# Kernel tuning notes

Hardware: AMD Instinct MI355X
Metric: run time of the kernel (lower is better)

Reference implementation:

```python
import jax, jax.numpy as jnp
import numpy as np

D = 256          # num_channels
H = 4            # num_heads
DH = D // H      # head dim
BN_EPS = 1e-5


def conv1x1(x, W, b):
    # x: [B, Cin, N], W: [Cout, Cin], b: [Cout] -> [B, Cout, N]
    return jnp.einsum('oc,bcn->bon', W, x) + b[None, :, None]


def bn_eval(x, gamma, beta):
    # eval-mode BatchNorm1d with running_mean=0, running_var=1
    scale = gamma / jnp.sqrt(1.0 + BN_EPS)
    return x * scale[None, :, None] + beta[None, :, None]


def setup_inputs() -> dict:
    key = jax.random.key(0)
    ks = jax.random.split(key, 16)
    B, N = 1, 4096
    s = 0.05
    inp = {
        'corr_feat_belief': jax.random.normal(ks[0], (B, D, N), dtype=jnp.float32),
        'spatial_compatibility': jax.random.uniform(ks[1], (B, N, N), dtype=jnp.float32),
        'Wq': jax.random.normal(ks[2], (D, D), dtype=jnp.float32) * s,
        'bq': jnp.zeros((D,), jnp.float32),
        'Wk': jax.random.normal(ks[3], (D, D), dtype=jnp.float32) * s,
        'bk': jnp.zeros((D,), jnp.float32),
        'Wv': jax.random.normal(ks[4], (D, D), dtype=jnp.float32) * s,
        'bv': jnp.zeros((D,), jnp.float32),
        'W1': jax.random.normal(ks[5], (D // 2, D), dtype=jnp.float32) * s,
        'b1': jnp.zeros((D // 2,), jnp.float32),
        'g1': jnp.ones((D // 2,), jnp.float32),
        'be1': jnp.zeros((D // 2,), jnp.float32),
        'W2': jax.random.normal(ks[6], (D // 2, D // 2), dtype=jnp.float32) * s,
        'b2': jnp.zeros((D // 2,), jnp.float32),
        'g2': jnp.ones((D // 2,), jnp.float32),
        'be2': jnp.zeros((D // 2,), jnp.float32),
        'W3': jax.random.normal(ks[7], (D, D // 2), dtype=jnp.float32) * s,
        'b3': jnp.zeros((D,), jnp.float32),
    }
    return inp


def reference(corr_feat_belief, spatial_compatibility, Wq, bq, Wk, bk, Wv, bv,
              W1, b1, g1, be1, W2, b2, g2, be2, W3, b3):
    x = corr_feat_belief                      # [B, D, N]
    B, _, N = x.shape
    # QKV conv1x1 projections, split heads -> [B, H, DH, N]
    Q = conv1x1(x, Wq, bq).reshape(B, H, DH, N)
    K = conv1x1(x, Wk, bk).reshape(B, H, DH, N)
    V = conv1x1(x, Wv, bv).reshape(B, H, DH, N)
    # attention scores [B, H, N, N], scaled
    att = jnp.einsum('bhco,bhci->bhoi', Q, K) / np.sqrt(DH).astype(np.float32)
    # multiplicative spatial-compatibility mask, softmax over keys
    weight = jax.nn.softmax(spatial_compatibility[:, None, :, :] * att, axis=-1)
    message = jnp.einsum('bhoi,bhci->bhco', weight, V).reshape(B, D, N)
    # message MLP: conv1x1 -> BN -> ReLU -> conv1x1 -> BN -> ReLU -> conv1x1
    h = jax.nn.relu(bn_eval(conv1x1(message, W1, b1), g1, be1))
    h = jax.nn.relu(bn_eval(conv1x1(h, W2, b2), g2, be2))
    h = conv1x1(h, W3, b3)
    return x + h
```

## Files before the change

kernel.cpp:

```cpp
#include <hip/hip_runtime.h>
#include <hip/hip_bf16.h>
#include <math.h>

#define D_CH   256
#define NHEAD  4
#define DHEAD  64
#define NPTS   4096
#define KSPLIT 8
#define KCHUNK (NPTS / KSPLIT)
#define BN_RSQ 0.99999500003749963f
#define HSTRIDE 262144

typedef __attribute__((ext_vector_type(4))) float f32x4;
typedef __attribute__((ext_vector_type(8))) short bf16x8;
typedef unsigned short ushort_t;

__device__ __forceinline__ ushort_t f2bf(float x) {
    unsigned int b = __float_as_uint(x);
    return (ushort_t)((b + 0x7FFF + ((b >> 16) & 1)) >> 16);
}
__device__ __forceinline__ float bf2f(ushort_t u) {
    return __uint_as_float(((unsigned int)u) << 16);
}
__device__ __forceinline__ unsigned cvt_pk(float lo, float hi) {
    unsigned r;
    asm("v_cvt_pk_bf16_f32 %0, %1, %2" : "=v"(r) : "v"(lo), "v"(hi));
    return r;
}

__global__ __launch_bounds__(256) void transpose_cast(
    const float* __restrict__ x, ushort_t* __restrict__ xT)
{
    __shared__ float xs[64][65];
    const int tid = threadIdx.x;
    const int n0 = blockIdx.x * 64, k0 = blockIdx.y * 64;
#pragma unroll
    for (int p = 0; p < 16; ++p) {
        int kk = p * 4 + (tid >> 6), nn = tid & 63;
        xs[kk][nn] = x[(size_t)(k0 + kk) * NPTS + n0 + nn];
    }
    __syncthreads();
#pragma unroll
    for (int p = 0; p < 16; ++p) {
        int nn = p * 4 + (tid >> 6), kk = tid & 63;
        xT[(size_t)(n0 + nn) * D_CH + k0 + kk] = f2bf(xs[kk][nn]);
    }
}

__device__ __forceinline__ void gemm_tile_body(
    const float* __restrict__ A, const ushort_t* __restrict__ Bt,
    int K, int m0, int n0, int l15, int lhi, f32x4 acc[2][2])
{
#pragma unroll
    for (int i = 0; i < 2; ++i)
#pragma unroll
        for (int j = 0; j < 2; ++j) acc[i][j] = (f32x4){0.f, 0.f, 0.f, 0.f};

    for (int k0 = 0; k0 < K; k0 += 32) {
        bf16x8 af[2], bfr[2];
#pragma unroll
        for (int mf = 0; mf < 2; ++mf) {
            const float* ap = A + (size_t)(m0 + mf * 16 + l15) * K + k0 + lhi * 8;
            float4 a0 = *(const float4*)ap;
            float4 a1 = *(const float4*)(ap + 4);
            unsigned* tp = (unsigned*)&af[mf];
            tp[0] = cvt_pk(a0.x, a0.y);
            tp[1] = cvt_pk(a0.z, a0.w);
            tp[2] = cvt_pk(a1.x, a1.y);
            tp[3] = cvt_pk(a1.z, a1.w);
        }
#pragma unroll
        for (int nf = 0; nf < 2; ++nf)
            bfr[nf] = *(const bf16x8*)&Bt[(size_t)(n0 + nf * 16 + l15) * K + k0 + lhi * 8];
#pragma unroll
        for (int mf = 0; mf < 2; ++mf)
#pragma unroll
            for (int nf = 0; nf < 2; ++nf)
                acc[mf][nf] = __builtin_amdgcn_mfma_f32_16x16x32_bf16(af[mf], bfr[nf], acc[mf][nf], 0, 0, 0);
    }
}

__global__ __launch_bounds__(256) void gemm_qkv(
    const float* __restrict__ Wq, const float* __restrict__ bq,
    const float* __restrict__ Wk, const float* __restrict__ bk,
    const float* __restrict__ Wv, const float* __restrict__ bv,
    const ushort_t* __restrict__ xT,
    ushort_t* __restrict__ Qf, ushort_t* __restrict__ Kf, ushort_t* __restrict__ Vf)
{
    const int tid = threadIdx.x;
    const int w = tid >> 6, lane = tid & 63, l15 = lane & 15, lhi = lane >> 4;
    const int wm = w >> 1, wn = w & 1;
    const int m0 = blockIdx.y * 64 + wm * 32;
    const int n0 = blockIdx.x * 64 + wn * 32;
    const int z = blockIdx.z;

    const float* A    = (z == 0) ? Wq : (z == 1) ? Wk : Wv;
    const float* bias = (z == 0) ? bq : (z == 1) ? bk : bv;
    ushort_t* dst     = (z == 0) ? Qf : (z == 1) ? Kf : Vf;
    const float scl   = (z == 0) ? 0.125f : 1.0f;

    f32x4 acc[2][2];
    gemm_tile_body(A, xT, D_CH, m0, n0, l15, lhi, acc);

#pragma unroll
    for (int mf = 0; mf < 2; ++mf) {
#pragma unroll
        for (int r = 0; r < 4; ++r) {
            int m = m0 + mf * 16 + lhi * 4 + r;
            int head = m >> 6, dch = m & 63;
            float bi = bias[m];
#pragma unroll
            for (int nf = 0; nf < 2; ++nf) {
                int n = n0 + nf * 16 + l15;
                float v = (acc[mf][nf][r] + bi) * scl;
                size_t idx;
                if (z < 2)
                    idx = (size_t)head * HSTRIDE + (size_t)(n >> 4) * 1024 + (dch >> 5) * 512
                        + (((dch >> 3) & 3) * 16 + (n & 15)) * 8 + (dch & 7);
                else
                    idx = (size_t)head * HSTRIDE + (size_t)(n >> 6) * 4096 + (dch >> 4) * 1024
                        + ((n >> 5) & 1) * 512 + (((n >> 3) & 3) * 16 + (dch & 15)) * 8 + (n & 7);
                dst[idx] = (ushort_t)(cvt_pk(v, v) & 0xFFFF);
            }
        }
    }
}

__global__ __launch_bounds__(256) void gemm_mfma32(
    const float* __restrict__ A, const ushort_t* __restrict__ Bt,
    void* __restrict__ Cout, int M, int N, int K,
    const float* __restrict__ bias, const float* __restrict__ gamma,
    const float* __restrict__ beta, int relu, const float* __restrict__ resid,
    int out_mode)
{
    const int tid = threadIdx.x;
    const int w = tid >> 6, lane = tid & 63, l15 = lane & 15, lhi = lane >> 4;
    const int wm = w >> 1, wn = w & 1;
    const int m0 = blockIdx.y * 32 + wm * 16;
    const int n0 = blockIdx.x * 64 + wn * 32;

    f32x4 acc[2];
#pragma unroll
    for (int j = 0; j < 2; ++j) acc[j] = (f32x4){0.f, 0.f, 0.f, 0.f};

    for (int k0 = 0; k0 < K; k0 += 32) {
        const float* ap = A + (size_t)(m0 + l15) * K + k0 + lhi * 8;
        float4 a0 = *(const float4*)ap;
        float4 a1 = *(const float4*)(ap + 4);
        bf16x8 af;
        unsigned* tp = (unsigned*)&af;
        tp[0] = cvt_pk(a0.x, a0.y);
        tp[1] = cvt_pk(a0.z, a0.w);
        tp[2] = cvt_pk(a1.x, a1.y);
        tp[3] = cvt_pk(a1.z, a1.w);
#pragma unroll
        for (int nf = 0; nf < 2; ++nf) {
            bf16x8 bfr = *(const bf16x8*)&Bt[(size_t)(n0 + nf * 16 + l15) * K + k0 + lhi * 8];
            acc[nf] = __builtin_amdgcn_mfma_f32_16x16x32_bf16(af, bfr, acc[nf], 0, 0, 0);
        }
    }

    float* Cf = (float*)Cout;
    ushort_t* Cu = (ushort_t*)Cout;
#pragma unroll
    for (int r = 0; r < 4; ++r) {
        int m = m0 + lhi * 4 + r;
        float bi = bias[m];
        float sc = 1.0f, sh = 0.0f;
        if (gamma) { sc = gamma[m] * BN_RSQ; sh = beta[m]; }
#pragma unroll
        for (int nf = 0; nf < 2; ++nf) {
            int n = n0 + nf * 16 + l15;
            float v = acc[nf][r] + bi;
            if (gamma) v = v * sc + sh;
            if (relu)  v = fmaxf(v, 0.0f);
            if (resid) v += resid[(size_t)m * N + n];
            if (out_mode == 0) Cf[(size_t)m * N + n] = v;
            else               Cu[(size_t)n * M + m] = (ushort_t)(cvt_pk(v, v) & 0xFFFF);
        }
    }
}

__device__ __forceinline__ void attn_tile(
    int kt, int ktn, const float* __restrict__ Sg,
    const ushort_t* __restrict__ Kh, const ushort_t* __restrict__ Vh,
    const bf16x8 (&qf)[2][2],
    ushort_t (* __restrict__ Sw)[72],
    f32x4 (&macc)[2][4], float (&lrun)[2],
    ushort_t (* __restrict__ Pw)[72], int l15, int lhi, int lane)
{
    f32x4 sr[8];
#pragma unroll
    for (int p = 0; p < 8; ++p)
        sr[p] = *(const f32x4*)&Sg[(size_t)p * 4 * NPTS + (size_t)ktn * 64];

    f32x4 sacc0[4], sacc1[4];
    __builtin_amdgcn_s_setprio(1);
#pragma unroll
    for (int kb = 0; kb < 4; ++kb) {
        const ushort_t* kp = Kh + (size_t)(kt * 4 + kb) * 1024 + lane * 8;
        bf16x8 kf0 = *(const bf16x8*)kp;
        bf16x8 kf1 = *(const bf16x8*)(kp + 512);
        f32x4 z0 = (f32x4){0.f, 0.f, 0.f, 0.f};
        z0 = __builtin_amdgcn_mfma_f32_16x16x32_bf16(kf0, qf[0][0], z0, 0, 0, 0);
        z0 = __builtin_amdgcn_mfma_f32_16x16x32_bf16(kf1, qf[0][1], z0, 0, 0, 0);
        sacc0[kb] = z0;
        f32x4 z1 = (f32x4){0.f, 0.f, 0.f, 0.f};
        z1 = __builtin_amdgcn_mfma_f32_16x16x32_bf16(kf0, qf[1][0], z1, 0, 0, 0);
        z1 = __builtin_amdgcn_mfma_f32_16x16x32_bf16(kf1, qf[1][1], z1, 0, 0, 0);
        sacc1[kb] = z1;
    }
    __builtin_amdgcn_s_setprio(0);

    bf16x8 vf[8];
    const ushort_t* vb = Vh + (size_t)kt * 4096 + lane * 8;
#pragma unroll
    for (int mm = 0; mm < 2; ++mm)
#pragma unroll
        for (int db = 0; db < 4; ++db)
            vf[mm * 4 + db] = *(const bf16x8*)(vb + db * 1024 + mm * 512);

    float ts0 = 0.0f, ts1 = 0.0f;
#pragma unroll
    for (int kb = 0; kb < 4; ++kb) {
        unsigned a0 = *(const unsigned*)&Sw[l15][kb * 16 + lhi * 4];
        unsigned a1 = *(const unsigned*)&Sw[l15][kb * 16 + lhi * 4 + 2];
        unsigned b0 = *(const unsigned*)&Sw[16 + l15][kb * 16 + lhi * 4];
        unsigned b1 = *(const unsigned*)&Sw[16 + l15][kb * 16 + lhi * 4 + 2];
        float p00 = __expf(sacc0[kb][0] * bf2f((ushort_t)(a0 & 0xFFFF)));
        float p01 = __expf(sacc0[kb][1] * bf2f((ushort_t)(a0 >> 16)));
        float p02 = __expf(sacc0[kb][2] * bf2f((ushort_t)(a1 & 0xFFFF)));
        float p03 = __expf(sacc0[kb][3] * bf2f((ushort_t)(a1 >> 16)));
        float p10 = __expf(sacc1[kb][0] * bf2f((ushort_t)(b0 & 0xFFFF)));
        float p11 = __expf(sacc1[kb][1] * bf2f((ushort_t)(b0 >> 16)));
        float p12 = __expf(sacc1[kb][2] * bf2f((ushort_t)(b1 & 0xFFFF)));
        float p13 = __expf(sacc1[kb][3] * bf2f((ushort_t)(b1 >> 16)));
        ts0 += (p00 + p01) + (p02 + p03);
        ts1 += (p10 + p11) + (p12 + p13);
        *(unsigned*)&Pw[l15][kb * 16 + lhi * 4]          = cvt_pk(p00, p01);
        *(unsigned*)&Pw[l15][kb * 16 + lhi * 4 + 2]      = cvt_pk(p02, p03);
        *(unsigned*)&Pw[16 + l15][kb * 16 + lhi * 4]     = cvt_pk(p10, p11);
        *(unsigned*)&Pw[16 + l15][kb * 16 + lhi * 4 + 2] = cvt_pk(p12, p13);
    }
    lrun[0] += ts0;
    lrun[1] += ts1;

#pragma unroll
    for (int p = 0; p < 8; ++p) {
        *(unsigned*)&Sw[p * 4 + lhi][l15 * 4]     = cvt_pk(sr[p][0], sr[p][1]);
        *(unsigned*)&Sw[p * 4 + lhi][l15 * 4 + 2] = cvt_pk(sr[p][2], sr[p][3]);
    }

    __builtin_amdgcn_s_setprio(1);
#pragma unroll
    for (int mm = 0; mm < 2; ++mm) {
        bf16x8 pf0 = *(const bf16x8*)&Pw[l15][mm * 32 + lhi * 8];
        bf16x8 pf1 = *(const bf16x8*)&Pw[16 + l15][mm * 32 + lhi * 8];
#pragma unroll
        for (int db = 0; db < 4; ++db) {
            macc[0][db] = __builtin_amdgcn_mfma_f32_16x16x32_bf16(vf[mm * 4 + db], pf0, macc[0][db], 0, 0, 0);
            macc[1][db] = __builtin_amdgcn_mfma_f32_16x16x32_bf16(vf[mm * 4 + db], pf1, macc[1][db], 0, 0, 0);
        }
    }
    __builtin_amdgcn_s_setprio(0);
}

__global__ __launch_bounds__(256, 3) void attn_mfma(
    const ushort_t* __restrict__ Qf, const ushort_t* __restrict__ Kf,
    const ushort_t* __restrict__ Vf, const float* __restrict__ S,
    ushort_t* __restrict__ pacc, float* __restrict__ pl)
{
    __shared__ __align__(16) ushort_t P_lds[4][32][72];
    __shared__ __align__(16) ushort_t S_lds[4][32][72];

    const int tid  = threadIdx.x;
    const int w    = tid >> 6;
    const int lane = tid & 63;
    const int l15  = lane & 15;
    const int lhi  = lane >> 4;
    const int h    = blockIdx.y;
    const int ks   = blockIdx.z;
    const int q0   = blockIdx.x * 128 + w * 32;
    const int ktb  = ks * (KCHUNK / 64);

    const ushort_t* Kh = Kf + (size_t)h * HSTRIDE;
    const ushort_t* Vh = Vf + (size_t)h * HSTRIDE;
    const float* Sg = S + (size_t)(q0 + lhi) * NPTS + l15 * 4;
    ushort_t (* __restrict__ Pw)[72] = P_lds[w];
    ushort_t (* __restrict__ Sw)[72] = S_lds[w];

    bf16x8 qf[2][2];
#pragma unroll
    for (int f = 0; f < 2; ++f) {
        const ushort_t* qp = Qf + (size_t)h * HSTRIDE
                           + (size_t)((q0 + f * 16) >> 4) * 1024 + lane * 8;
        qf[f][0] = *(const bf16x8*)qp;
        qf[f][1] = *(const bf16x8*)(qp + 512);
    }

    f32x4 macc[2][4];
#pragma unroll
    for (int f = 0; f < 2; ++f)
#pragma unroll
        for (int db = 0; db < 4; ++db) macc[f][db] = (f32x4){0.f, 0.f, 0.f, 0.f};
    float lrun[2] = {0.0f, 0.0f};

    {
#pragma unroll
        for (int p = 0; p < 8; ++p) {
            f32x4 t = *(const f32x4*)&Sg[(size_t)p * 4 * NPTS + (size_t)ktb * 64];
            *(unsigned*)&Sw[p * 4 + lhi][l15 * 4]     = cvt_pk(t[0], t[1]);
            *(unsigned*)&Sw[p * 4 + lhi][l15 * 4 + 2] = cvt_pk(t[2], t[3]);
        }
    }

    for (int kt = ktb; kt < ktb + 8; ++kt) {
        const int ktn = (kt + 1 < ktb + 8) ? kt + 1 : ktb;
        attn_tile(kt, ktn, Sg, Kh, Vh, qf, Sw, macc, lrun, Pw, l15, lhi, lane);
    }

#pragma unroll
    for (int f = 0; f < 2; ++f) {
        lrun[f] += __shfl_xor(lrun[f], 16);
        lrun[f] += __shfl_xor(lrun[f], 32);
    }

    const size_t pb = ((size_t)ks * NHEAD + h) * NPTS;
#pragma unroll
    for (int f = 0; f < 2; ++f) {
        ushort_t* prow = pacc + (pb + q0 + f * 16 + l15) * DHEAD;
#pragma unroll
        for (int db = 0; db < 4; ++db) {
            *(unsigned*)&prow[db * 16 + lhi * 4]     = cvt_pk(macc[f][db][0], macc[f][db][1]);
            *(unsigned*)&prow[db * 16 + lhi * 4 + 2] = cvt_pk(macc[f][db][2], macc[f][db][3]);
        }
    }
    if (lane < 16) {
        pl[pb + q0 + lane]      = lrun[0];
        pl[pb + q0 + 16 + lane] = lrun[1];
    }
}

__global__ __launch_bounds__(256) void attn_merge(
    const ushort_t* __restrict__ pacc, const float* __restrict__ pl,
    ushort_t* __restrict__ msgT)
{
    const int h = blockIdx.y;
    const int q = blockIdx.x * 64 + (threadIdx.x >> 2);
    const int d0 = (threadIdx.x & 3) * 16;

    float ls = 0.0f;
#pragma unroll
    for (int ks = 0; ks < KSPLIT; ++ks)
        ls += pl[((size_t)ks * NHEAD + h) * NPTS + q];
    float inv = 1.0f / ls;

    float out[16];
#pragma unroll
    for (int j = 0; j < 16; ++j) out[j] = 0.0f;
#pragma unroll
    for (int ks = 0; ks < KSPLIT; ++ks) {
        const ushort_t* ap = pacc + (((size_t)ks * NHEAD + h) * NPTS + q) * DHEAD + d0;
        bf16x8 v0 = *(const bf16x8*)ap;
        bf16x8 v1 = *(const bf16x8*)(ap + 8);
#pragma unroll
        for (int j = 0; j < 8; ++j) {
            out[j]     += bf2f((ushort_t)v0[j]);
            out[8 + j] += bf2f((ushort_t)v1[j]);
        }
    }
    unsigned o[8];
#pragma unroll
    for (int j = 0; j < 4; ++j) {
        o[j]     = cvt_pk(out[j * 2] * inv,     out[j * 2 + 1] * inv);
        o[4 + j] = cvt_pk(out[8 + j * 2] * inv, out[8 + j * 2 + 1] * inv);
    }
    unsigned* op = (unsigned*)(msgT + (size_t)q * D_CH + h * DHEAD + d0);
    *(uint4*)op       = make_uint4(o[0], o[1], o[2], o[3]);
    *(uint4*)(op + 4) = make_uint4(o[4], o[5], o[6], o[7]);
}

extern "C" void kernel_launch(void* const* d_in, const int* in_sizes, int n_in,
                              void* d_out, int out_size, void* d_ws, size_t ws_size,
                              hipStream_t stream) {
    const float* x  = (const float*)d_in[0];
    const float* S  = (const float*)d_in[1];
    const float* Wq = (const float*)d_in[2];
    const float* bq = (const float*)d_in[3];
    const float* Wk = (const float*)d_in[4];
    const float* bk = (const float*)d_in[5];
    const float* Wv = (const float*)d_in[6];
    const float* bv = (const float*)d_in[7];
    const float* W1 = (const float*)d_in[8];
    const float* b1 = (const float*)d_in[9];
    const float* g1 = (const float*)d_in[10];
    const float* be1= (const float*)d_in[11];
    const float* W2 = (const float*)d_in[12];
    const float* b2 = (const float*)d_in[13];
    const float* g2 = (const float*)d_in[14];
    const float* be2= (const float*)d_in[15];
    const float* W3 = (const float*)d_in[16];
    const float* b3 = (const float*)d_in[17];

    char* ws = (char*)d_ws;
    const size_t MB = 1024 * 1024;
    ushort_t* xT   = (ushort_t*)(ws);
    ushort_t* Qf   = (ushort_t*)(ws + 2 * MB);
    ushort_t* Kf   = (ushort_t*)(ws + 4 * MB);
    ushort_t* Vf   = (ushort_t*)(ws + 6 * MB);
    ushort_t* pacc = (ushort_t*)(ws + 8 * MB);
    float*    pl   = (float*)   (ws + 24 * MB);
    ushort_t* msgT = (ushort_t*)(ws + 25 * MB);
    ushort_t* h1T  = (ushort_t*)(ws + 27 * MB);
    ushort_t* h2T  = (ushort_t*)(ws + 28 * MB);

    transpose_cast<<<dim3(64, 4), 256, 0, stream>>>(x, xT);
    gemm_qkv<<<dim3(64, 4, 3), 256, 0, stream>>>(Wq, bq, Wk, bk, Wv, bv, xT, Qf, Kf, Vf);

    attn_mfma<<<dim3(32, NHEAD, KSPLIT), 256, 0, stream>>>(Qf, Kf, Vf, S, pacc, pl);
    attn_merge<<<dim3(64, NHEAD), 256, 0, stream>>>(pacc, pl, msgT);

    gemm_mfma32<<<dim3(64, 4), 256, 0, stream>>>(W1, msgT, h1T, 128, NPTS, 256, b1, g1, be1, 1, nullptr, 3);
    gemm_mfma32<<<dim3(64, 4), 256, 0, stream>>>(W2, h1T, h2T, 128, NPTS, 128, b2, g2, be2, 1, nullptr, 3);
    gemm_mfma32<<<dim3(64, 8), 256, 0, stream>>>(W3, h2T, d_out, 256, NPTS, 128, b3, nullptr, nullptr, 0, x, 0);
}
```

Baseline: 101.7 us.

## Fuse three MLP conv1x1 GEMMs into a single per-point-block kernel

Replaces three separate GEMM launches for the message MLP with one kernel in which each block processes 32 points through all three layers. Intermediate activations are still written to global scratch, but they are read back by the same block after a block barrier, so they stay cache-local. This removes two kernel launches and inter-kernel gaps, at the cost of only 128 blocks and serialized layers within a block.

```diff
diff --git a/kernel.cpp b/kernel.cpp
--- a/kernel.cpp
+++ b/kernel.cpp
@@ -122,61 +122,6 @@
                         + ((n >> 5) & 1) * 512 + (((n >> 3) & 3) * 16 + (dch & 15)) * 8 + (n & 7);
                 dst[idx] = (ushort_t)(cvt_pk(v, v) & 0xFFFF);
             }
-        }
-    }
-}
-
-__global__ __launch_bounds__(256) void gemm_mfma32(
-    const float* __restrict__ A, const ushort_t* __restrict__ Bt,
-    void* __restrict__ Cout, int M, int N, int K,
-    const float* __restrict__ bias, const float* __restrict__ gamma,
-    const float* __restrict__ beta, int relu, const float* __restrict__ resid,
-    int out_mode)
-{
-    const int tid = threadIdx.x;
-    const int w = tid >> 6, lane = tid & 63, l15 = lane & 15, lhi = lane >> 4;
-    const int wm = w >> 1, wn = w & 1;
-    const int m0 = blockIdx.y * 32 + wm * 16;
-    const int n0 = blockIdx.x * 64 + wn * 32;
-
-    f32x4 acc[2];
-#pragma unroll
-    for (int j = 0; j < 2; ++j) acc[j] = (f32x4){0.f, 0.f, 0.f, 0.f};
-
-    for (int k0 = 0; k0 < K; k0 += 32) {
-        const float* ap = A + (size_t)(m0 + l15) * K + k0 + lhi * 8;
-        float4 a0 = *(const float4*)ap;
-        float4 a1 = *(const float4*)(ap + 4);
-        bf16x8 af;
-        unsigned* tp = (unsigned*)&af;
-        tp[0] = cvt_pk(a0.x, a0.y);
-        tp[1] = cvt_pk(a0.z, a0.w);
-        tp[2] = cvt_pk(a1.x, a1.y);
-        tp[3] = cvt_pk(a1.z, a1.w);
-#pragma unroll
-        for (int nf = 0; nf < 2; ++nf) {
-            bf16x8 bfr = *(const bf16x8*)&Bt[(size_t)(n0 + nf * 16 + l15) * K + k0 + lhi * 8];
-            acc[nf] = __builtin_amdgcn_mfma_f32_16x16x32_bf16(af, bfr, acc[nf], 0, 0, 0);
-        }
-    }
-
-    float* Cf = (float*)Cout;
-    ushort_t* Cu = (ushort_t*)Cout;
-#pragma unroll
-    for (int r = 0; r < 4; ++r) {
-        int m = m0 + lhi * 4 + r;
-        float bi = bias[m];
-        float sc = 1.0f, sh = 0.0f;
-        if (gamma) { sc = gamma[m] * BN_RSQ; sh = beta[m]; }
-#pragma unroll
-        for (int nf = 0; nf < 2; ++nf) {
-            int n = n0 + nf * 16 + l15;
-            float v = acc[nf][r] + bi;
-            if (gamma) v = v * sc + sh;
-            if (relu)  v = fmaxf(v, 0.0f);
-            if (resid) v += resid[(size_t)m * N + n];
-            if (out_mode == 0) Cf[(size_t)m * N + n] = v;
-            else               Cu[(size_t)n * M + m] = (ushort_t)(cvt_pk(v, v) & 0xFFFF);
         }
     }
 }
@@ -378,6 +323,78 @@
     unsigned* op = (unsigned*)(msgT + (size_t)q * D_CH + h * DHEAD + d0);
     *(uint4*)op       = make_uint4(o[0], o[1], o[2], o[3]);
     *(uint4*)(op + 4) = make_uint4(o[4], o[5], o[6], o[7]);
+}
+
+__global__ __launch_bounds__(256) void mlp_fused(
+    const ushort_t* __restrict__ msgT,
+    const float* __restrict__ W1, const float* __restrict__ b1,
+    const float* __restrict__ g1, const float* __restrict__ be1,
+    const float* __restrict__ W2, const float* __restrict__ b2,
+    const float* __restrict__ g2, const float* __restrict__ be2,
+    const float* __restrict__ W3, const float* __restrict__ b3,
+    const float* __restrict__ x, float* __restrict__ out,
+    ushort_t* __restrict__ h1T, ushort_t* __restrict__ h2T)
+{
+    const int tid = threadIdx.x;
+    const int w = tid >> 6, lane = tid & 63, l15 = lane & 15, lhi = lane >> 4;
+    const int nblk = blockIdx.x * 32;
+
+    {
+        f32x4 acc[2][2];
+        gemm_tile_body(W1, msgT + (size_t)nblk * D_CH, D_CH, w * 32, 0, l15, lhi, acc);
+#pragma unroll
+        for (int mf = 0; mf < 2; ++mf)
+#pragma unroll
+            for (int r = 0; r < 4; ++r) {
+                int m = w * 32 + mf * 16 + lhi * 4 + r;
+                float bi = b1[m], sc = g1[m] * BN_RSQ, sh = be1[m];
+#pragma unroll
+                for (int nf = 0; nf < 2; ++nf) {
+                    int n = nf * 16 + l15;
+                    float v = fmaxf((acc[mf][nf][r] + bi) * sc + sh, 0.0f);
+                    h1T[(size_t)(nblk + n) * 128 + m] = (ushort_t)(cvt_pk(v, v) & 0xFFFF);
+                }
+            }
+    }
+    __syncthreads();
+
+    {
+        f32x4 acc[2][2];
+        gemm_tile_body(W2, h1T + (size_t)nblk * 128, 128, w * 32, 0, l15, lhi, acc);
+#pragma unroll
+        for (int mf = 0; mf < 2; ++mf)
+#pragma unroll
+            for (int r = 0; r < 4; ++r) {
+                int m = w * 32 + mf * 16 + lhi * 4 + r;
+                float bi = b2[m], sc = g2[m] * BN_RSQ, sh = be2[m];
+#pragma unroll
+                for (int nf = 0; nf < 2; ++nf) {
+                    int n = nf * 16 + l15;
+                    float v = fmaxf((acc[mf][nf][r] + bi) * sc + sh, 0.0f);
+                    h2T[(size_t)(nblk + n) * 128 + m] = (ushort_t)(cvt_pk(v, v) & 0xFFFF);
+                }
+            }
+    }
+    __syncthreads();
+
+#pragma unroll
+    for (int half = 0; half < 2; ++half) {
+        f32x4 acc[2][2];
+        const int m0 = w * 64 + half * 32;
+        gemm_tile_body(W3, h2T + (size_t)nblk * 128, 128, m0, 0, l15, lhi, acc);
+#pragma unroll
+        for (int mf = 0; mf < 2; ++mf)
+#pragma unroll
+            for (int r = 0; r < 4; ++r) {
+                int m = m0 + mf * 16 + lhi * 4 + r;
+                float bi = b3[m];
+#pragma unroll
+                for (int nf = 0; nf < 2; ++nf) {
+                    int n = nblk + nf * 16 + l15;
+                    out[(size_t)m * NPTS + n] = acc[mf][nf][r] + bi + x[(size_t)m * NPTS + n];
+                }
+            }
+    }
 }
 
 extern "C" void kernel_launch(void* const* d_in, const int* in_sizes, int n_in,
@@ -420,7 +437,6 @@
     attn_mfma<<<dim3(32, NHEAD, KSPLIT), 256, 0, stream>>>(Qf, Kf, Vf, S, pacc, pl);
     attn_merge<<<dim3(64, NHEAD), 256, 0, stream>>>(pacc, pl, msgT);
 
-    gemm_mfma32<<<dim3(64, 4), 256, 0, stream>>>(W1, msgT, h1T, 128, NPTS, 256, b1, g1, be1, 1, nullptr, 3);
-    gemm_mfma32<<<dim3(64, 4), 256, 0, stream>>>(W2, h1T, h2T, 128, NPTS, 128, b2, g2, be2, 1, nullptr, 3);
-    gemm_mfma32<<<dim3(64, 8), 256, 0, stream>>>(W3, h2T, d_out, 256, NPTS, 128, b3, nullptr, nullptr, 0, x, 0);
-}
+    mlp_fused<<<dim3(128), 256, 0, stream>>>(msgT,
+        W1, b1, g1, be1, W2, b2, g2, be2, W3, b3, x, (float*)d_out, h1T, h2T);
+}
```

After: 98.38 us. -3.3%, faster.
